# Kernel tuning notes

Hardware: AMD Instinct MI355X
Metric: run time of the kernel (lower is better)

The kernel has to match this reference:

```python
import jax, jax.numpy as jnp
import numpy as np

B, S, H = 16, 384, 768
DK, ESS, WHOLE = 64, 6, 8
HEADER = WHOLE + 1
NL_RGAT = 2


def _sinusoidal_pos(seq_len, dim):
    pos = np.arange(seq_len)[:, None]
    j = np.arange(dim)[None, :]
    enc = pos / np.power(10000.0, 2 * (j // 2) / dim)
    sent = dim // 2
    out = np.zeros((seq_len, dim), dtype=np.float32)
    out[:, :sent] = np.sin(enc[:, 0::2])
    out[:, sent:] = np.cos(enc[:, 1::2])
    return jnp.asarray(out)[None, None]  # [1,1,S,dim]


def _rope(pos, x):
    sin, cos = jnp.split(pos, 2, axis=-1)
    sin_pos = jnp.stack([sin, sin], -1).reshape(pos.shape)
    cos_pos = jnp.stack([cos, cos], -1).reshape(pos.shape)
    rot = jnp.stack([-x[..., 1::2], x[..., 0::2]], -1).reshape(x.shape)
    return x * cos_pos + rot * sin_pos


def _mlp(x, rep_w, rep_b, sc_w, sc_b):
    return jax.nn.relu(x @ rep_w.T + rep_b) @ sc_w.T + sc_b


def _heads(y, mask, n_heads):
    b, s = y.shape[:2]
    return (y * mask).reshape(b, s, n_heads, DK).transpose(0, 2, 1, 3)


def _shaking(M, rows, cols):
    # M: [B,nH,S,S] -> [B,P,nH]; upper triangle (incl diag), row-major
    return M[:, :, rows, cols].transpose(0, 2, 1)


def _layernorm(x, eps=1e-5):
    m = x.mean(-1, keepdims=True)
    v = ((x - m) ** 2).mean(-1, keepdims=True)
    return (x - m) * jax.lax.rsqrt(v + eps)


def setup_inputs() -> dict:
    key = jax.random.key(0)
    ks = jax.random.split(key, 32)
    n = lambda i, shape: jax.random.normal(ks[i], shape, dtype=jnp.float32) * 0.02
    ig = (H + DK * HEADER) // 2          # 672
    ip = (2 * H + DK * ESS) // 2          # 960
    return dict(
        seq_hiddens=jax.random.normal(ks[0], (B, S, H), dtype=jnp.float32),
        attention_mask=jnp.ones((B, S, 1), dtype=jnp.float32),
        wq4gt_w=n(1, (DK, H)), wq4gt_b=n(2, (DK,)),
        wk4gt_w=n(3, (DK, H)), wk4gt_b=n(4, (DK,)),
        wq4g_rep_w=n(5, (ig, H)), wq4g_rep_b=n(6, (ig,)),
        wq4g_sc_w=n(7, (DK * HEADER, ig)), wq4g_sc_b=n(8, (DK * HEADER,)),
        wk4g_rep_w=n(9, (ig, H)), wk4g_rep_b=n(10, (ig,)),
        wk4g_sc_w=n(11, (DK * HEADER, ig)), wk4g_sc_b=n(12, (DK * HEADER,)),
        rgat_w=n(13, (NL_RGAT, HEADER, H, H)),
        wq4t_w=n(14, (DK, 2 * H)), wq4t_b=n(15, (DK,)),
        wk4t_w=n(16, (DK, 2 * H)), wk4t_b=n(17, (DK,)),
        wq_rep_w=n(18, (ip, 2 * H)), wq_rep_b=n(19, (ip,)),
        wq_sc_w=n(20, (DK * ESS, ip)), wq_sc_b=n(21, (DK * ESS,)),
        wk_rep_w=n(22, (ip, 2 * H)), wk_rep_b=n(23, (ip,)),
        wk_sc_w=n(24, (DK * ESS, ip)), wk_sc_b=n(25, (DK * ESS,)),
    )


def reference(seq_hiddens, attention_mask,
              wq4gt_w, wq4gt_b, wk4gt_w, wk4gt_b,
              wq4g_rep_w, wq4g_rep_b, wq4g_sc_w, wq4g_sc_b,
              wk4g_rep_w, wk4g_rep_b, wk4g_sc_w, wk4g_sc_b,
              rgat_w,
              wq4t_w, wq4t_b, wk4t_w, wk4t_b,
              wq_rep_w, wq_rep_b, wq_sc_w, wq_sc_b,
              wk_rep_w, wk_rep_b, wk_sc_w, wk_sc_b):
    pos = _sinusoidal_pos(S, DK)
    rows, cols = np.triu_indices(S)
    inv = 1.0 / np.sqrt(DK).astype(np.float32)
    mask = attention_mask
    x = seq_hiddens

    # ----- graph layer (graph_stack_num = 1) -----
    tsq = _rope(pos, _heads(x @ wq4gt_w.T + wq4gt_b, mask, 1))
    tsk = _rope(pos, _heads(x @ wk4gt_w.T + wk4gt_b, mask, 1))
    thr_g = jax.nn.relu(_shaking(jnp.einsum('bhqd,bhkd->bhqk', tsq, tsk) * inv, rows, cols))

    q = _rope(pos, _heads(_mlp(x, wq4g_rep_w, wq4g_rep_b, wq4g_sc_w, wq4g_sc_b), mask, HEADER))
    k = _rope(pos, _heads(_mlp(x, wk4g_rep_w, wk4g_rep_b, wk4g_sc_w, wk4g_sc_b), mask, HEADER))
    score = jnp.einsum('bhqd,bhkd->bhqk', q, k) * inv  # [B,HEADER,S,S]
    sc_g = _shaking(score[:, :WHOLE], rows, cols)

    upper = jnp.triu(score, 1)
    diag = jnp.triu(score, 0) - upper
    att = upper + jnp.swapaxes(upper, -1, -2) + diag  # symmetric
    adj = jax.nn.softmax(att, -1) * (att != 0)

    feat = x
    for l in range(NL_RGAT):
        hr = jnp.einsum('bsh,roh->brso', feat, rgat_w[l])           # per-relation Linear (no bias)
        agg = jax.nn.relu(jnp.einsum('brst,brto->brso', adj, hr))   # adjacency bmm + ReLU
        feat = _layernorm(jax.nn.relu(agg.sum(1)) / HEADER)         # (dropout is eval-identity)

    # ----- prediction head -----
    inp = jnp.concatenate([seq_hiddens, feat], -1)  # [B,S,2H]
    tq = _rope(pos, _heads(inp @ wq4t_w.T + wq4t_b, mask, 1))
    tk = _rope(pos, _heads(inp @ wk4t_w.T + wk4t_b, mask, 1))
    thr_p = jax.nn.relu(_shaking(jnp.einsum('bhqd,bhkd->bhqk', tq, tk) * inv, rows, cols))

    qp = _rope(pos, _heads(_mlp(inp, wq_rep_w, wq_rep_b, wq_sc_w, wq_sc_b), mask, ESS))
    kp = _rope(pos, _heads(_mlp(inp, wk_rep_w, wk_rep_b, wk_sc_w, wk_sc_b), mask, ESS))
    sc_p = _shaking(jnp.einsum('bhqd,bhkd->bhqk', qp, kp) * inv, rows, cols)

    # concat all shaking outputs along last dim: [B, S(S+1)/2, ESS+1+WHOLE+1]
    return jnp.concatenate([sc_p, thr_p, sc_g, thr_g], -1)
```

## Files before the change

kernel.cpp:

```cpp
#include <hip/hip_runtime.h>
#include <math.h>

typedef unsigned short ushort_t;
typedef __attribute__((ext_vector_type(8))) short short8;
typedef __attribute__((ext_vector_type(4))) float f32x4;

constexpr int B = 16, S = 384, H = 768;
constexpr int BS = B * S;
constexpr long long PAIRS = (long long)S * (S + 1) / 2;
constexpr float INV = 0.125f;

__device__ __forceinline__ ushort_t f2bf(float f) {
  unsigned int u = __float_as_uint(f);
  u += 0x7FFF + ((u >> 16) & 1);
  return (ushort_t)(u >> 16);
}
__device__ __forceinline__ float bf2f(ushort_t u) {
  return __uint_as_float(((unsigned int)u) << 16);
}

__device__ __forceinline__ void glds16(const ushort_t* g, ushort_t* l) {
  __builtin_amdgcn_global_load_lds(
      (const __attribute__((address_space(1))) unsigned int*)g,
      (__attribute__((address_space(3))) unsigned int*)l, 16, 0, 0);
}

__global__ __launch_bounds__(256) void setup_kernel(
    float* tab,
    const float* g_repq, const float* g_repk, const float* g_gtq, const float* g_gtk,
    const float* p_repq, const float* p_repk, const float* p_gtq, const float* p_gtk,
    const float* g_scq, const float* g_sck, const float* p_scq, const float* p_sck,
    float* bqkg, float* bqkp, float* bscg, float* bscp) {
  int b = blockIdx.x;
  if (b < 48) {
    int s = b * 8 + (threadIdx.x >> 5);
    int i = threadIdx.x & 31;
    double ang = (double)s / pow(10000.0, (double)i / 32.0);
    tab[s * 64 + 2 * i]     = (float)cos(ang);
    tab[s * 64 + 2 * i + 1] = (float)sin(ang);
  } else {
    int t = (b - 48) * 256 + threadIdx.x;
    if (t < 1472)
      bqkg[t] = t < 672 ? g_repq[t] : t < 1344 ? g_repk[t - 672]
              : t < 1408 ? g_gtq[t - 1344] : g_gtk[t - 1408];
    if (t < 2048)
      bqkp[t] = t < 960 ? p_repq[t] : t < 1920 ? p_repk[t - 960]
              : t < 1984 ? p_gtq[t - 1920] : p_gtk[t - 1984];
    if (t < 1152) bscg[t] = t < 576 ? g_scq[t] : g_sck[t - 576];
    if (t < 768)  bscp[t] = t < 384 ? p_scq[t] : p_sck[t - 384];
  }
}

constexpr int NJOBS = 14;
struct CvtJobs {
  const float* src[NJOBS];
  ushort_t* dst[NJOBS];
  int n_real[NJOBS];
  int n_tot[NJOBS];
  int blk_off[NJOBS + 1];
};
__global__ __launch_bounds__(256) void cvt_jobs_kernel(CvtJobs J) {
  int blk = blockIdx.x;
  int j = 0;
  while (j < NJOBS - 1 && blk >= J.blk_off[j + 1]) ++j;
  int i4 = (blk - J.blk_off[j]) * 256 + threadIdx.x;
  if (i4 * 4 >= J.n_tot[j]) return;
  ushort4 o;
  if (i4 * 4 < J.n_real[j]) {
    float4 v = ((const float4*)J.src[j])[i4];
    o = make_ushort4(f2bf(v.x), f2bf(v.y), f2bf(v.z), f2bf(v.w));
  } else {
    o = make_ushort4(0, 0, 0, 0);
  }
  ((ushort4*)J.dst[j])[i4] = o;
}

template <int ACT, int CMODE, int SWZ>
__global__ __launch_bounds__(256) void gemm_nt_mfma(
    const ushort_t* __restrict__ A, const ushort_t* __restrict__ W,
    const float* __restrict__ bias, void* __restrict__ Cv,
    ushort_t* __restrict__ pl, ushort_t* __restrict__ qd,
    ushort_t* __restrict__ kd, int cbase, int nsplit,
    int N, int K, int lda, int ldw, int ldc, float alpha, int nh,
    long long sAb, long long sAh, long long sWb, long long sWh,
    long long sCb, long long sCh,
    const float* __restrict__ mask, const float* __restrict__ tab, int biasN) {
  constexpr int SHSZ = (CMODE == 2 || CMODE == 8) ? 17408 : 16384;
  __shared__ __align__(16) ushort_t SH[SHSZ];
  int bx = blockIdx.x, by = blockIdx.y, bz = blockIdx.z;
  if (SWZ) {
    const int nx = gridDim.x, ny = gridDim.y;
    const int nwg = nx * ny * gridDim.z;
    const int hw = bx + nx * (by + ny * bz);
    int l = (hw & 7) * (nwg >> 3) + (hw >> 3);
    const int pz = l / (nx * ny);
    int l2 = l - pz * (nx * ny);
    const int GM = 8;
    const int band = l2 / (GM * nx);
    const int rem = l2 - band * (GM * nx);
    const int gm = (ny - band * GM < GM) ? (ny - band * GM) : GM;
    bx = rem / gm;
    by = band * GM + (rem - bx * gm);
    bz = pz;
  }
  const int zb = bz / nh, zh = bz - zb * nh;
  A += zb * sAb + zh * sAh;
  W += zb * sWb + zh * sWh;
  const int t = threadIdx.x;
  int m0, n0;
  if (CMODE == 3 || CMODE == 8) {
    const int ti = (bx < 3) ? 0 : (bx < 5 ? 1 : 2);
    const int tj = (bx < 3) ? bx : (bx < 5 ? bx - 2 : 2);
    m0 = ti * 128; n0 = tj * 128;
  } else {
    m0 = by * 128; n0 = bx * 128;
  }
  const int lane = t & 63, wid = t >> 6;
  const int wr = wid >> 1, wc = wid & 1;
  const int lrow = lane & 15, lk = lane >> 4;
  const int srow = t >> 2, sch = (t & 3) * 8;
  const ushort_t* Ag = A + (size_t)(m0 + srow) * lda + sch;
  const ushort_t* Wg = W + (size_t)(n0 + srow) * ldw + sch;
  const size_t a64 = (size_t)64 * lda, w64 = (size_t)64 * ldw;

  f32x4 acc[4][4];
#pragma unroll
  for (int i = 0; i < 4; ++i)
#pragma unroll
    for (int j = 0; j < 4; ++j) acc[i][j] = (f32x4){0.f, 0.f, 0.f, 0.f};

  auto stage = [&](int k0, int buf) {
    const int ao = buf * 4096, bo = 8192 + buf * 4096;
    glds16(Ag + k0, &SH[ao + t * 8]);
    glds16(Ag + k0 + a64, &SH[ao + 2048 + t * 8]);
    glds16(Wg + k0, &SH[bo + t * 8]);
    glds16(Wg + k0 + w64, &SH[bo + 2048 + t * 8]);
  };

  const int nk = K >> 5;
  stage(0, 0);
  for (int s = 0; s < nk; ++s) {
    __syncthreads();
    if (s + 1 < nk) stage((s + 1) << 5, (s + 1) & 1);
    const int ao = (s & 1) * 4096, bo = 8192 + (s & 1) * 4096;
    short8 av[4], bv[4];
#pragma unroll
    for (int i = 0; i < 4; ++i) {
      av[i] = *(const short8*)&SH[ao + (wr * 64 + i * 16 + lrow) * 32 + lk * 8];
      bv[i] = *(const short8*)&SH[bo + (wc * 64 + i * 16 + lrow) * 32 + lk * 8];
    }
#pragma unroll
    for (int i = 0; i < 4; ++i)
#pragma unroll
      for (int j = 0; j < 4; ++j)
        acc[i][j] = __builtin_amdgcn_mfma_f32_16x16x32_bf16(av[i], bv[j],
                                                            acc[i][j], 0, 0, 0);
  }

  if (CMODE == 2) {
    __syncthreads();
    const int bb = m0 / S;
    ushort_t* Cb = (ushort_t*)Cv + (size_t)bb * sCb;
    const int s_base = m0 - bb * S;
#pragma unroll
    for (int i = 0; i < 4; ++i) {
      const int sl = wr * 64 + i * 16 + lk * 4;
#pragma unroll
      for (int j = 0; j < 4; ++j) {
        const int nl = wc * 64 + j * 16 + lrow;
        ushort4 o = make_ushort4(f2bf(acc[i][j][0]), f2bf(acc[i][j][1]),
                                 f2bf(acc[i][j][2]), f2bf(acc[i][j][3]));
        *(ushort4*)&SH[nl * 136 + sl] = o;
      }
    }
    __syncthreads();
#pragma unroll
    for (int it = 0; it < 8; ++it) {
      const int row = it * 16 + wid * 4 + lk;
      ushort_t* dst = Cb + (size_t)(n0 + row) * ldc + s_base + lrow * 8;
      *(short8*)dst = *(const short8*)&SH[row * 136 + lrow * 8];
    }
  } else if (CMODE == 3) {
    ushort_t* plc = pl + ((size_t)(cbase + zh) * B + zb) * PAIRS;
#pragma unroll
    for (int j = 0; j < 4; ++j) {
      const int n = n0 + wc * 64 + j * 16 + lrow;
#pragma unroll
      for (int i = 0; i < 4; ++i) {
#pragma unroll
        for (int e = 0; e < 4; ++e) {
          const int m = m0 + wr * 64 + i * 16 + lk * 4 + e;
          if (n >= m) {
            long long p = (long long)m * S - (long long)m * (m - 1) / 2 + (n - m);
            float v = alpha * acc[i][j][e];
            if (ACT == 1) v = fmaxf(v, 0.f);
            plc[p] = f2bf(v);
          }
        }
      }
    }
  } else if (CMODE == 5) {
    ushort_t* Cq = qd + (size_t)zh * sCh;
    const float* bz2 = bias + (size_t)zh * biasN;
#pragma unroll
    for (int j = 0; j < 4; ++j) {
      const int n = n0 + wc * 64 + j * 16 + lrow;
      const float vb = (n < N) ? bz2[n] : 0.f;
      const int d = n & 63;
      const int ti2 = d & ~1;
#pragma unroll
      for (int i = 0; i < 4; ++i) {
#pragma unroll
        for (int e = 0; e < 4; ++e) {
          const int m = m0 + wr * 64 + i * 16 + lk * 4 + e;
          const int s = m % S;
          float v = (n < N) ? (acc[i][j][e] + vb) : 0.f;
          float pv = __shfl_xor(v, 1);
          float c = tab[s * 64 + ti2], sn = tab[s * 64 + ti2 + 1];
          float o = (d & 1) ? (v * c + pv * sn) : (v * c - pv * sn);
          o *= mask[m];
          if (n < N) Cq[(size_t)m * ldc + n] = f2bf(o);
        }
      }
    }
  } else if (CMODE == 6) {
    ushort_t* Cu = (ushort_t*)Cv;
#pragma unroll
    for (int j = 0; j < 4; ++j) {
      const int n = n0 + wc * 64 + j * 16 + lrow;
      const float vb = (n < N) ? bias[n] : 0.f;
#pragma unroll
      for (int i = 0; i < 4; ++i) {
#pragma unroll
        for (int e = 0; e < 4; ++e) {
          const int m = m0 + wr * 64 + i * 16 + lk * 4 + e;
          float v = (n < N) ? (acc[i][j][e] + vb) : 0.f;
          float pv = __shfl_xor(v, 1);
          if (n < nsplit) {
            Cu[(size_t)m * ldc + n] = f2bf(fmaxf(v, 0.f));
          } else if (n < N) {
            const int d = n - nsplit;
            const int dd = d & 63;
            const int ti2 = dd & ~1;
            const int s = m % S;
            float c = tab[s * 64 + ti2], sn = tab[s * 64 + ti2 + 1];
            float o = (dd & 1) ? (v * c + pv * sn) : (v * c - pv * sn);
            o *= mask[m];
            if (d < 64) qd[(size_t)m * 64 + dd] = f2bf(o);
            else        kd[(size_t)m * 64 + dd] = f2bf(o);
          }
        }
      }
    }
  } else if (CMODE == 8) {
    ushort_t* Cu = (ushort_t*)Cv + zb * sCb + zh * sCh;
    ushort_t* plc = pl + ((size_t)(cbase + zh) * B + zb) * PAIRS;
    const bool diag = (m0 == n0);
#pragma unroll
    for (int j = 0; j < 4; ++j) {
      const int n = n0 + wc * 64 + j * 16 + lrow;
#pragma unroll
      for (int i = 0; i < 4; ++i) {
#pragma unroll
        for (int e = 0; e < 4; ++e) {
          const int m = m0 + wr * 64 + i * 16 + lk * 4 + e;
          float v = alpha * acc[i][j][e];
          ushort_t vb = f2bf(v);
          if (!diag || n >= m) Cu[(size_t)m * ldc + n] = vb;
          if (zh < 8 && n >= m) {
            long long p = (long long)m * S - (long long)m * (m - 1) / 2 + (n - m);
            plc[p] = vb;
          }
        }
      }
    }
    __syncthreads();
#pragma unroll
    for (int i = 0; i < 4; ++i) {
      const int sl = wr * 64 + i * 16 + lk * 4;
#pragma unroll
      for (int j = 0; j < 4; ++j) {
        const int nl = wc * 64 + j * 16 + lrow;
        ushort4 o4 = make_ushort4(f2bf(alpha * acc[i][j][0]),
                                  f2bf(alpha * acc[i][j][1]),
                                  f2bf(alpha * acc[i][j][2]),
                                  f2bf(alpha * acc[i][j][3]));
        *(ushort4*)&SH[nl * 136 + sl] = o4;
      }
    }
    __syncthreads();
#pragma unroll
    for (int it = 0; it < 8; ++it) {
      const int rowN = it * 16 + wid * 4 + lk;
      const int colM = lrow * 8;
      if (!diag) {
        *(short8*)&Cu[(size_t)(n0 + rowN) * ldc + m0 + colM] =
            *(const short8*)&SH[rowN * 136 + colM];
      } else {
#pragma unroll
        for (int q = 0; q < 8; ++q)
          if (rowN > colM + q)
            Cu[(size_t)(n0 + rowN) * ldc + m0 + colM + q] =
                SH[rowN * 136 + colM + q];
      }
    }
  }
}

__global__ __launch_bounds__(256) void adj_bmm_kernel(
    const ushort_t* __restrict__ adjb, const ushort_t* __restrict__ hrt,
    ushort_t* __restrict__ Q0, ushort_t* __restrict__ Q1,
    ushort_t* __restrict__ Q2, ushort_t* __restrict__ Q3,
    ushort_t* __restrict__ Q4) {
  __shared__ __align__(16) ushort_t As[2][128 * 32];
  __shared__ __align__(16) ushort_t Bs[2][128 * 32];
  int bx = blockIdx.x, by = blockIdx.y, bz = blockIdx.z;
  {
    int nx = gridDim.x, ny = gridDim.y;
    int nwg = nx * ny * gridDim.z;
    int flat = bx + nx * (by + ny * bz);
    int l = (flat & 7) * (nwg >> 3) + (flat >> 3);
    bx = l % nx; l /= nx; by = l % ny; bz = l / ny;
  }
  const int b = bz / 5, rg = bz - b * 5;
  ushort_t* Q = (rg == 0) ? Q0 : (rg == 1) ? Q1 : (rg == 2) ? Q2
              : (rg == 3) ? Q3 : Q4;
  const int rel0 = (rg < 4) ? rg * 2 : 8;
  const int nsteps = (rg < 4) ? 24 : 12;
  const int t = threadIdx.x;
  const int m0 = by * 128, n0 = bx * 128;
  const int lane = t & 63, wid = t >> 6;
  const int wr = wid >> 1, wc = wid & 1;
  const int lrow = lane & 15, lk = lane >> 4;
  const int srow = t >> 2, sch = (t & 3) * 8;

  const ushort_t* adjA =
      adjb + ((size_t)(b * 9 + rel0) * S + m0 + srow) * S + sch;
  const ushort_t* hrA =
      hrt + ((size_t)(b * 9 + rel0) * H + n0 + srow) * S + sch;

  float mac[4][4][4];
#pragma unroll
  for (int i = 0; i < 4; ++i)
#pragma unroll
    for (int j = 0; j < 4; ++j)
#pragma unroll
      for (int e = 0; e < 4; ++e) mac[i][j][e] = 0.f;

  f32x4 acc[4][4];
#pragma unroll
  for (int i = 0; i < 4; ++i)
#pragma unroll
    for (int j = 0; j < 4; ++j) acc[i][j] = (f32x4){0.f, 0.f, 0.f, 0.f};

  auto stage = [&](int s, int buf) {
    const int rr = s / 12;
    const int k0 = (s - rr * 12) * 32;
    const ushort_t* Ag = adjA + (size_t)rr * S * S + k0;
    const ushort_t* Wg = hrA + (size_t)rr * H * S + k0;
    glds16(Ag, &As[buf][t * 8]);
    glds16(Ag + 64 * S, &As[buf][2048 + t * 8]);
    glds16(Wg, &Bs[buf][t * 8]);
    glds16(Wg + 64 * S, &Bs[buf][2048 + t * 8]);
  };

  stage(0, 0);
  for (int s = 0; s < nsteps; ++s) {
    __syncthreads();
    if (s + 1 < nsteps) stage(s + 1, (s + 1) & 1);
    const int buf = s & 1;
    short8 av[4], bv[4];
#pragma unroll
    for (int i = 0; i < 4; ++i) {
      av[i] = *(const short8*)&As[buf][(wr * 64 + i * 16 + lrow) * 32 + lk * 8];
      bv[i] = *(const short8*)&Bs[buf][(wc * 64 + i * 16 + lrow) * 32 + lk * 8];
    }
#pragma unroll
    for (int i = 0; i < 4; ++i)
#pragma unroll
      for (int j = 0; j < 4; ++j)
        acc[i][j] = __builtin_amdgcn_mfma_f32_16x16x32_bf16(av[i], bv[j],
                                                            acc[i][j], 0, 0, 0);
    if ((s % 12) == 11) {
#pragma unroll
      for (int i = 0; i < 4; ++i)
#pragma unroll
        for (int j = 0; j < 4; ++j) {
#pragma unroll
          for (int e = 0; e < 4; ++e)
            mac[i][j][e] += fmaxf(acc[i][j][e], 0.f);
          acc[i][j] = (f32x4){0.f, 0.f, 0.f, 0.f};
        }
    }
  }

#pragma unroll
  for (int i = 0; i < 4; ++i)
#pragma unroll
    for (int j = 0; j < 4; ++j)
#pragma unroll
      for (int e = 0; e < 4; ++e) {
        const int m = m0 + wr * 64 + i * 16 + lk * 4 + e;
        const int n = n0 + wc * 64 + j * 16 + lrow;
        Q[((size_t)b * S + m) * H + n] = f2bf(mac[i][j][e]);
      }
}

__global__ __launch_bounds__(128) void softmax_mask_kernel(
    const ushort_t* __restrict__ Mt, ushort_t* __restrict__ adjb) {
  __shared__ float red[128];
  int row = blockIdx.x;
  const ushort_t* r = Mt + (size_t)row * S;
  ushort_t* o = adjb + (size_t)row * S;
  int t = threadIdx.x;
  const bool act = t < 96;
  float v[4];
  float mx = -INFINITY;
  if (act) {
    ushort4 u = ((const ushort4*)r)[t];
    v[0] = bf2f(u.x); v[1] = bf2f(u.y); v[2] = bf2f(u.z); v[3] = bf2f(u.w);
    mx = fmaxf(fmaxf(v[0], v[1]), fmaxf(v[2], v[3]));
  }
  red[t] = mx; __syncthreads();
  for (int off2 = 64; off2 > 0; off2 >>= 1) {
    if (t < off2) red[t] = fmaxf(red[t], red[t + off2]);
    __syncthreads();
  }
  mx = red[0]; __syncthreads();
  float e4[4], s = 0.f;
  if (act) {
#pragma unroll
    for (int q = 0; q < 4; ++q) { e4[q] = expf(v[q] - mx); s += e4[q]; }
  }
  red[t] = s; __syncthreads();
  for (int off2 = 64; off2 > 0; off2 >>= 1) {
    if (t < off2) red[t] += red[t + off2];
    __syncthreads();
  }
  float invs = 1.f / red[0];
  if (act) {
    ushort4 ou;
    ou.x = f2bf((v[0] != 0.f) ? e4[0] * invs : 0.f);
    ou.y = f2bf((v[1] != 0.f) ? e4[1] * invs : 0.f);
    ou.z = f2bf((v[2] != 0.f) ? e4[2] * invs : 0.f);
    ou.w = f2bf((v[3] != 0.f) ? e4[3] * invs : 0.f);
    ((ushort4*)o)[t] = ou;
  }
}

__global__ __launch_bounds__(256) void ln_finalize_kernel(
    const ushort_t* __restrict__ Q0, const ushort_t* __restrict__ Q1,
    const ushort_t* __restrict__ Q2, const ushort_t* __restrict__ Q3,
    const ushort_t* __restrict__ Q4, const ushort_t* __restrict__ xb,
    ushort_t* __restrict__ inp) {
  __shared__ float red[256];
  int row = blockIdx.x;
  const size_t base = (size_t)row * H;
  ushort_t* xrow = inp + (size_t)row * (2 * H);
  ushort_t* fb = xrow + H;
  int t = threadIdx.x;
  float v[3];
  float s = 0.f;
#pragma unroll
  for (int q = 0; q < 3; ++q) {
    size_t ix = base + t + q * 256;
    v[q] = (bf2f(Q0[ix]) + bf2f(Q1[ix]) + bf2f(Q2[ix]) + bf2f(Q3[ix]) +
            bf2f(Q4[ix])) / 9.0f;
    s += v[q];
  }
  red[t] = s; __syncthreads();
#pragma unroll
  for (int q = 0; q < 3; ++q)
    xrow[t + q * 256] = xb[base + t + q * 256];
  for (int off2 = 128; off2 > 0; off2 >>= 1) {
    if (t < off2) red[t] += red[t + off2];
    __syncthreads();
  }
  float mean = red[0] / (float)H; __syncthreads();
  float s2 = 0.f;
#pragma unroll
  for (int q = 0; q < 3; ++q) { float d = v[q] - mean; s2 += d * d; }
  red[t] = s2; __syncthreads();
  for (int off2 = 128; off2 > 0; off2 >>= 1) {
    if (t < off2) red[t] += red[t + off2];
    __syncthreads();
  }
  float var = red[0] / (float)H;
  float rs = rsqrtf(var + 1e-5f);
#pragma unroll
  for (int q = 0; q < 3; ++q)
    fb[t + q * 256] = f2bf((v[q] - mean) * rs);
}

__global__ __launch_bounds__(256) void gather16_kernel(
    const ushort_t* __restrict__ plA, const ushort_t* __restrict__ plB,
    float* __restrict__ out) {
  int idx = blockIdx.x * 256 + threadIdx.x;
  if (idx >= (int)(B * PAIRS)) return;
  const size_t PLN = (size_t)B * PAIRS;
  float v[16];
#pragma unroll
  for (int ch = 0; ch < 7; ++ch)  v[ch] = bf2f(plA[(size_t)ch * PLN + idx]);
#pragma unroll
  for (int ch = 7; ch < 16; ++ch) v[ch] = bf2f(plB[(size_t)(ch - 7) * PLN + idx]);
  float4* dst = (float4*)(out + (size_t)idx * 16);
#pragma unroll
  for (int q = 0; q < 4; ++q)
    dst[q] = make_float4(v[4 * q], v[4 * q + 1], v[4 * q + 2], v[4 * q + 3]);
}

extern "C" void kernel_launch(void* const* d_in, const int* in_sizes, int n_in,
                              void* d_out, int out_size, void* d_ws, size_t ws_size,
                              hipStream_t stream) {
  (void)in_sizes; (void)n_in; (void)out_size; (void)ws_size;
  const float* x          = (const float*)d_in[0];
  const float* mask       = (const float*)d_in[1];
  const float* wq4gt_w    = (const float*)d_in[2];
  const float* wq4gt_b    = (const float*)d_in[3];
  const float* wk4gt_w    = (const float*)d_in[4];
  const float* wk4gt_b    = (const float*)d_in[5];
  const float* wq4g_rep_w = (const float*)d_in[6];
  const float* wq4g_rep_b = (const float*)d_in[7];
  const float* wq4g_sc_w  = (const float*)d_in[8];
  const float* wq4g_sc_b  = (const float*)d_in[9];
  const float* wk4g_rep_w = (const float*)d_in[10];
  const float* wk4g_rep_b = (const float*)d_in[11];
  const float* wk4g_sc_w  = (const float*)d_in[12];
  const float* wk4g_sc_b  = (const float*)d_in[13];
  const float* rgat_w     = (const float*)d_in[14];
  const float* wq4t_w     = (const float*)d_in[15];
  const float* wq4t_b     = (const float*)d_in[16];
  const float* wk4t_w     = (const float*)d_in[17];
  const float* wk4t_b     = (const float*)d_in[18];
  const float* wq_rep_w   = (const float*)d_in[19];
  const float* wq_rep_b   = (const float*)d_in[20];
  const float* wq_sc_w    = (const float*)d_in[21];
  const float* wq_sc_b    = (const float*)d_in[22];
  const float* wk_rep_w   = (const float*)d_in[23];
  const float* wk_rep_b   = (const float*)d_in[24];
  const float* wk_sc_w    = (const float*)d_in[25];
  const float* wk_sc_b    = (const float*)d_in[26];
  float* out = (float*)d_out;

  char* wsb = (char*)d_ws;
  size_t off = 0;
  auto af = [&](size_t n) { float* p = (float*)(wsb + off);
                            off += ((n * 4 + 255) & ~(size_t)255); return p; };
  auto au = [&](size_t n) { ushort_t* p = (ushort_t*)(wsb + off);
                            off += ((n * 2 + 255) & ~(size_t)255); return p; };

  float* t_rope = af(24576);
  float* t_scg  = af((size_t)B * 9 * S * S);
  float* t_acc  = af((size_t)BS * H);
  ushort_t* xb    = au((size_t)BS * H);
  ushort_t* inpb  = au((size_t)BS * 2 * H);
  ushort_t* repb  = au((size_t)BS * 1920);
  ushort_t* qb    = au((size_t)BS * 576);
  ushort_t* kb    = au((size_t)BS * 576);
  ushort_t* adjb  = au((size_t)B * 9 * S * S);
  ushort_t* plB   = au((size_t)9 * B * PAIRS);
  ushort_t* wqkg  = au(1179648);
  ushort_t* wqkp  = au(3145728);
  ushort_t* wq4g_scb = au(430080);
  ushort_t* wk4g_scb = au(430080);
  ushort_t* wq_scb   = au(368640);
  ushort_t* wk_scb   = au(368640);
  ushort_t* rgatb    = au(10616832);
  float* bqkg = af(1472);
  float* bqkp = af(2048);
  float* bscg = af(1152);
  float* bscp = af(768);

  ushort_t* scg_u = (ushort_t*)t_scg;
  ushort_t* hr_t  = (ushort_t*)t_scg;
  ushort_t* plA   = rgatb;
  ushort_t* Q0 = (ushort_t*)t_acc;
  ushort_t* Q1 = Q0 + (size_t)BS * H;
  ushort_t* Q2 = repb;
  ushort_t* Q3 = Q2 + (size_t)BS * H;
  ushort_t* Q4 = qb;

  setup_kernel<<<56, 256, 0, stream>>>(
      t_rope,
      wq4g_rep_b, wk4g_rep_b, wq4gt_b, wk4gt_b,
      wq_rep_b, wk_rep_b, wq4t_b, wk4t_b,
      wq4g_sc_b, wk4g_sc_b, wq_sc_b, wk_sc_b,
      bqkg, bqkp, bscg, bscp);

  {
    CvtJobs J;
    const float* srcs[NJOBS] = {wq4g_rep_w, wk4g_rep_w, wq4gt_w, wk4gt_w,
                                wq_rep_w, wk_rep_w, wq4t_w, wk4t_w,
                                wq4g_sc_w, wk4g_sc_w, wq_sc_w, wk_sc_w,
                                rgat_w, x};
    ushort_t* dsts[NJOBS] = {wqkg, wqkg + 516096, wqkg + 1032192, wqkg + 1081344,
                             wqkp, wqkp + 1474560, wqkp + 2949120, wqkp + 3047424,
                             wq4g_scb, wk4g_scb, wq_scb, wk_scb,
                             rgatb, xb};
    int nreal[NJOBS] = {516096, 516096, 49152, 49152,
                        1474560, 1474560, 98304, 98304,
                        387072, 387072, 368640, 368640,
                        10616832, 4718592};
    int ntot[NJOBS]  = {516096, 516096, 49152, 98304,
                        1474560, 1474560, 98304, 98304,
                        430080, 430080, 368640, 368640,
                        10616832, 4718592};
    int acc_blk = 0;
    for (int j = 0; j < NJOBS; ++j) {
      J.src[j] = srcs[j]; J.dst[j] = dsts[j];
      J.n_real[j] = nreal[j]; J.n_tot[j] = ntot[j];
      J.blk_off[j] = acc_blk;
      acc_blk += (ntot[j] + 1023) / 1024;
    }
    J.blk_off[NJOBS] = acc_blk;
    cvt_jobs_kernel<<<acc_blk, 256, 0, stream>>>(J);
  }

  gemm_nt_mfma<0, 6, 1><<<dim3(12, 48, 1), 256, 0, stream>>>(
      xb, wqkg, bqkg, repb, nullptr, qb, kb, 0, 1344,
      1472, 768, 768, 768, 1344, 1.f, 1, 0, 0, 0, 0, 0, 0,
      mask, t_rope, 0);
  gemm_nt_mfma<1, 3, 1><<<dim3(6, 1, B), 256, 0, stream>>>(
      qb, kb, nullptr, nullptr, plB, nullptr, nullptr, 8, 0,
      S, 64, 64, 64, 0, INV, 1,
      (long long)S * 64, 0, (long long)S * 64, 0, 0, 0,
      nullptr, nullptr, 0);

  gemm_nt_mfma<0, 5, 1><<<dim3(5, 48, 2), 256, 0, stream>>>(
      repb, wq4g_scb, bscg, nullptr, nullptr, qb, nullptr, 0, 0,
      576, 672, 1344, 672, 576, 1.f, 2,
      0, 672, 0, 430080, 0, (long long)BS * 576,
      mask, t_rope, 576);
  gemm_nt_mfma<0, 8, 1><<<dim3(6, 1, B * 9), 256, 0, stream>>>(
      qb, kb, nullptr, scg_u, plB, nullptr, nullptr, 0, 0,
      S, 64, 576, 576, S, INV, 9,
      (long long)S * 576, 64, (long long)S * 576, 64,
      (long long)9 * S * S, (long long)S * S,
      nullptr, nullptr, 0);
  softmax_mask_kernel<<<B * 9 * S, 128, 0, stream>>>(scg_u, adjb);

  for (int l = 0; l < 2; ++l) {
    const ushort_t* fsrc = (l == 0) ? xb : inpb + H;
    const int flda = (l == 0) ? H : 2 * H;
    gemm_nt_mfma<0, 2, 1><<<dim3(54, 48, 1), 256, 0, stream>>>(
        fsrc, rgatb + (size_t)l * 9 * H * H, nullptr, hr_t, nullptr, nullptr,
        nullptr, 0, 0,
        9 * H, H, flda, H, S, 1.f, 1, 0, 0, 0, 0, (long long)9 * H * S, 0,
        nullptr, nullptr, 0);
    adj_bmm_kernel<<<dim3(6, 3, B * 5), 256, 0, stream>>>(
        adjb, hr_t, Q0, Q1, Q2, Q3, Q4);
    ln_finalize_kernel<<<BS, 256, 0, stream>>>(Q0, Q1, Q2, Q3, Q4, xb, inpb);
  }

  gemm_nt_mfma<0, 6, 1><<<dim3(16, 48, 1), 256, 0, stream>>>(
      inpb, wqkp, bqkp, repb, nullptr, qb, kb, 0, 1920,
      2048, 1536, 1536, 1536, 1920, 1.f, 1, 0, 0, 0, 0, 0, 0,
      mask, t_rope, 0);
  gemm_nt_mfma<1, 3, 1><<<dim3(6, 1, B), 256, 0, stream>>>(
      qb, kb, nullptr, nullptr, plA, nullptr, nullptr, 6, 0,
      S, 64, 64, 64, 0, INV, 1,
      (long long)S * 64, 0, (long long)S * 64, 0, 0, 0,
      nullptr, nullptr, 0);

  gemm_nt_mfma<0, 5, 1><<<dim3(3, 48, 2), 256, 0, stream>>>(
      repb, wq_scb, bscp, nullptr, nullptr, qb, nullptr, 0, 0,
      384, 960, 1920, 960, 384, 1.f, 2,
      0, 960, 0, 368640, 0, (long long)BS * 384,
      mask, t_rope, 384);
  gemm_nt_mfma<0, 3, 1><<<dim3(6, 1, B * 6), 256, 0, stream>>>(
      qb, qb + (size_t)BS * 384, nullptr, nullptr, plA, nullptr, nullptr, 0, 0,
      S, 64, 384, 384, 0, INV, 6,
      (long long)S * 384, 64, (long long)S * 384, 64, 0, 0,
      nullptr, nullptr, 0);

  gather16_kernel<<<(int)((B * PAIRS + 255) / 256), 256, 0, stream>>>(plA, plB, out);
}
```

Baseline: 654.0 us.

## Merge setup into convert kernel and co-launch independent small GEMMs

Folds the RoPE-table and bias-packing setup into the weight-conversion kernel so both run as one launch. Redirects the global-token q/k projections to spare buffers so the small triangular score GEMM can share a launch with the independent sc-projection GEMM, through a new dual-dispatch kernel driven by a flat block index. This cuts launch count and lets the under-filled 96-block GEMM overlap with the larger one. In exchange, kernel arguments now go through a struct and the merged kernels may use more registers or LDS.

Result: faster. 637.6 us (-2.5%).

```diff
diff --git a/kernel.cpp b/kernel.cpp
--- a/kernel.cpp
+++ b/kernel.cpp
@@ -23,32 +23,6 @@
   __builtin_amdgcn_global_load_lds(
       (const __attribute__((address_space(1))) unsigned int*)g,
       (__attribute__((address_space(3))) unsigned int*)l, 16, 0, 0);
-}
-
-__global__ __launch_bounds__(256) void setup_kernel(
-    float* tab,
-    const float* g_repq, const float* g_repk, const float* g_gtq, const float* g_gtk,
-    const float* p_repq, const float* p_repk, const float* p_gtq, const float* p_gtk,
-    const float* g_scq, const float* g_sck, const float* p_scq, const float* p_sck,
-    float* bqkg, float* bqkp, float* bscg, float* bscp) {
-  int b = blockIdx.x;
-  if (b < 48) {
-    int s = b * 8 + (threadIdx.x >> 5);
-    int i = threadIdx.x & 31;
-    double ang = (double)s / pow(10000.0, (double)i / 32.0);
-    tab[s * 64 + 2 * i]     = (float)cos(ang);
-    tab[s * 64 + 2 * i + 1] = (float)sin(ang);
-  } else {
-    int t = (b - 48) * 256 + threadIdx.x;
-    if (t < 1472)
-      bqkg[t] = t < 672 ? g_repq[t] : t < 1344 ? g_repk[t - 672]
-              : t < 1408 ? g_gtq[t - 1344] : g_gtk[t - 1408];
-    if (t < 2048)
-      bqkp[t] = t < 960 ? p_repq[t] : t < 1920 ? p_repk[t - 960]
-              : t < 1984 ? p_gtq[t - 1920] : p_gtk[t - 1984];
-    if (t < 1152) bscg[t] = t < 576 ? g_scq[t] : g_sck[t - 576];
-    if (t < 768)  bscp[t] = t < 384 ? p_scq[t] : p_sck[t - 384];
-  }
 }
 
 constexpr int NJOBS = 14;
@@ -59,8 +33,34 @@
   int n_tot[NJOBS];
   int blk_off[NJOBS + 1];
 };
-__global__ __launch_bounds__(256) void cvt_jobs_kernel(CvtJobs J) {
+__global__ __launch_bounds__(256) void cvt_setup_kernel(
+    CvtJobs J, int cvtBlocks, float* tab,
+    const float* g_repq, const float* g_repk, const float* g_gtq, const float* g_gtk,
+    const float* p_repq, const float* p_repk, const float* p_gtq, const float* p_gtk,
+    const float* g_scq, const float* g_sck, const float* p_scq, const float* p_sck,
+    float* bqkg, float* bqkp, float* bscg, float* bscp) {
   int blk = blockIdx.x;
+  if (blk >= cvtBlocks) {
+    int b = blk - cvtBlocks;
+    if (b < 48) {
+      int s = b * 8 + (threadIdx.x >> 5);
+      int i = threadIdx.x & 31;
+      double ang = (double)s / pow(10000.0, (double)i / 32.0);
+      tab[s * 64 + 2 * i]     = (float)cos(ang);
+      tab[s * 64 + 2 * i + 1] = (float)sin(ang);
+    } else {
+      int t = (b - 48) * 256 + threadIdx.x;
+      if (t < 1472)
+        bqkg[t] = t < 672 ? g_repq[t] : t < 1344 ? g_repk[t - 672]
+                : t < 1408 ? g_gtq[t - 1344] : g_gtk[t - 1408];
+      if (t < 2048)
+        bqkp[t] = t < 960 ? p_repq[t] : t < 1920 ? p_repk[t - 960]
+                : t < 1984 ? p_gtq[t - 1920] : p_gtk[t - 1984];
+      if (t < 1152) bscg[t] = t < 576 ? g_scq[t] : g_sck[t - 576];
+      if (t < 768)  bscp[t] = t < 384 ? p_scq[t] : p_sck[t - 384];
+    }
+    return;
+  }
   int j = 0;
   while (j < NJOBS - 1 && blk >= J.blk_off[j + 1]) ++j;
   int i4 = (blk - J.blk_off[j]) * 256 + threadIdx.x;
@@ -75,24 +75,24 @@
   ((ushort4*)J.dst[j])[i4] = o;
 }
 
-template <int ACT, int CMODE, int SWZ>
-__global__ __launch_bounds__(256) void gemm_nt_mfma(
-    const ushort_t* __restrict__ A, const ushort_t* __restrict__ W,
-    const float* __restrict__ bias, void* __restrict__ Cv,
-    ushort_t* __restrict__ pl, ushort_t* __restrict__ qd,
-    ushort_t* __restrict__ kd, int cbase, int nsplit,
-    int N, int K, int lda, int ldw, int ldc, float alpha, int nh,
-    long long sAb, long long sAh, long long sWb, long long sWh,
-    long long sCb, long long sCh,
-    const float* __restrict__ mask, const float* __restrict__ tab, int biasN) {
+struct GemmArgs {
+  const ushort_t* A; const ushort_t* W; const float* bias; void* Cv;
+  ushort_t* pl; ushort_t* qd; ushort_t* kd; int cbase, nsplit;
+  int N, K, lda, ldw, ldc; float alpha; int nh;
+  long long sAb, sAh, sWb, sWh, sCb, sCh;
+  const float* mask; const float* tab; int biasN;
+  int nx, ny, nz;
+};
+
+template <int ACT, int CMODE>
+__device__ void gemm_body(const GemmArgs g, int flat) {
   constexpr int SHSZ = (CMODE == 2 || CMODE == 8) ? 17408 : 16384;
   __shared__ __align__(16) ushort_t SH[SHSZ];
-  int bx = blockIdx.x, by = blockIdx.y, bz = blockIdx.z;
-  if (SWZ) {
-    const int nx = gridDim.x, ny = gridDim.y;
-    const int nwg = nx * ny * gridDim.z;
-    const int hw = bx + nx * (by + ny * bz);
-    int l = (hw & 7) * (nwg >> 3) + (hw >> 3);
+  const int nx = g.nx, ny = g.ny;
+  int bx, by, bz;
+  {
+    const int nwg = nx * ny * g.nz;
+    int l = (flat & 7) * (nwg >> 3) + (flat >> 3);
     const int pz = l / (nx * ny);
     int l2 = l - pz * (nx * ny);
     const int GM = 8;
@@ -103,9 +103,9 @@
     by = band * GM + (rem - bx * gm);
     bz = pz;
   }
-  const int zb = bz / nh, zh = bz - zb * nh;
-  A += zb * sAb + zh * sAh;
-  W += zb * sWb + zh * sWh;
+  const int zb = bz / g.nh, zh = bz - zb * g.nh;
+  const ushort_t* A = g.A + zb * g.sAb + zh * g.sAh;
+  const ushort_t* W = g.W + zb * g.sWb + zh * g.sWh;
   const int t = threadIdx.x;
   int m0, n0;
   if (CMODE == 3 || CMODE == 8) {
@@ -119,6 +119,7 @@
   const int wr = wid >> 1, wc = wid & 1;
   const int lrow = lane & 15, lk = lane >> 4;
   const int srow = t >> 2, sch = (t & 3) * 8;
+  const int lda = g.lda, ldw = g.ldw, ldc = g.ldc;
   const ushort_t* Ag = A + (size_t)(m0 + srow) * lda + sch;
   const ushort_t* Wg = W + (size_t)(n0 + srow) * ldw + sch;
   const size_t a64 = (size_t)64 * lda, w64 = (size_t)64 * ldw;
@@ -137,7 +138,7 @@
     glds16(Wg + k0 + w64, &SH[bo + 2048 + t * 8]);
   };
 
-  const int nk = K >> 5;
+  const int nk = g.K >> 5;
   stage(0, 0);
   for (int s = 0; s < nk; ++s) {
     __syncthreads();
@@ -160,7 +161,7 @@
   if (CMODE == 2) {
     __syncthreads();
     const int bb = m0 / S;
-    ushort_t* Cb = (ushort_t*)Cv + (size_t)bb * sCb;
+    ushort_t* Cb = (ushort_t*)g.Cv + (size_t)bb * g.sCb;
     const int s_base = m0 - bb * S;
 #pragma unroll
     for (int i = 0; i < 4; ++i) {
@@ -181,7 +182,7 @@
       *(short8*)dst = *(const short8*)&SH[row * 136 + lrow * 8];
     }
   } else if (CMODE == 3) {
-    ushort_t* plc = pl + ((size_t)(cbase + zh) * B + zb) * PAIRS;
+    ushort_t* plc = g.pl + ((size_t)(g.cbase + zh) * B + zb) * PAIRS;
 #pragma unroll
     for (int j = 0; j < 4; ++j) {
       const int n = n0 + wc * 64 + j * 16 + lrow;
@@ -192,7 +193,7 @@
           const int m = m0 + wr * 64 + i * 16 + lk * 4 + e;
           if (n >= m) {
             long long p = (long long)m * S - (long long)m * (m - 1) / 2 + (n - m);
-            float v = alpha * acc[i][j][e];
+            float v = g.alpha * acc[i][j][e];
             if (ACT == 1) v = fmaxf(v, 0.f);
             plc[p] = f2bf(v);
           }
@@ -200,12 +201,12 @@
       }
     }
   } else if (CMODE == 5) {
-    ushort_t* Cq = qd + (size_t)zh * sCh;
-    const float* bz2 = bias + (size_t)zh * biasN;
+    ushort_t* Cq = g.qd + (size_t)zh * g.sCh;
+    const float* bz2 = g.bias + (size_t)zh * g.biasN;
 #pragma unroll
     for (int j = 0; j < 4; ++j) {
       const int n = n0 + wc * 64 + j * 16 + lrow;
-      const float vb = (n < N) ? bz2[n] : 0.f;
+      const float vb = (n < g.N) ? bz2[n] : 0.f;
       const int d = n & 63;
       const int ti2 = d & ~1;
 #pragma unroll
@@ -214,47 +215,47 @@
         for (int e = 0; e < 4; ++e) {
           const int m = m0 + wr * 64 + i * 16 + lk * 4 + e;
           const int s = m % S;
-          float v = (n < N) ? (acc[i][j][e] + vb) : 0.f;
+          float v = (n < g.N) ? (acc[i][j][e] + vb) : 0.f;
           float pv = __shfl_xor(v, 1);
-          float c = tab[s * 64 + ti2], sn = tab[s * 64 + ti2 + 1];
+          float c = g.tab[s * 64 + ti2], sn = g.tab[s * 64 + ti2 + 1];
           float o = (d & 1) ? (v * c + pv * sn) : (v * c - pv * sn);
-          o *= mask[m];
-          if (n < N) Cq[(size_t)m * ldc + n] = f2bf(o);
+          o *= g.mask[m];
+          if (n < g.N) Cq[(size_t)m * ldc + n] = f2bf(o);
         }
       }
     }
   } else if (CMODE == 6) {
-    ushort_t* Cu = (ushort_t*)Cv;
+    ushort_t* Cu = (ushort_t*)g.Cv;
 #pragma unroll
     for (int j = 0; j < 4; ++j) {
       const int n = n0 + wc * 64 + j * 16 + lrow;
-      const float vb = (n < N) ? bias[n] : 0.f;
+      const float vb = (n < g.N) ? g.bias[n] : 0.f;
 #pragma unroll
       for (int i = 0; i < 4; ++i) {
 #pragma unroll
         for (int e = 0; e < 4; ++e) {
           const int m = m0 + wr * 64 + i * 16 + lk * 4 + e;
-          float v = (n < N) ? (acc[i][j][e] + vb) : 0.f;
+          float v = (n < g.N) ? (acc[i][j][e] + vb) : 0.f;
           float pv = __shfl_xor(v, 1);
-          if (n < nsplit) {
+          if (n < g.nsplit) {
             Cu[(size_t)m * ldc + n] = f2bf(fmaxf(v, 0.f));
-          } else if (n < N) {
-            const int d = n - nsplit;
+          } else if (n < g.N) {
+            const int d = n - g.nsplit;
             const int dd = d & 63;
             const int ti2 = dd & ~1;
             const int s = m % S;
-            float c = tab[s * 64 + ti2], sn = tab[s * 64 + ti2 + 1];
+            float c = g.tab[s * 64 + ti2], sn = g.tab[s * 64 + ti2 + 1];
             float o = (dd & 1) ? (v * c + pv * sn) : (v * c - pv * sn);
-            o *= mask[m];
-            if (d < 64) qd[(size_t)m * 64 + dd] = f2bf(o);
-            else        kd[(size_t)m * 64 + dd] = f2bf(o);
+            o *= g.mask[m];
+            if (d < 64) g.qd[(size_t)m * 64 + dd] = f2bf(o);
+            else        g.kd[(size_t)m * 64 + dd] = f2bf(o);
           }
         }
       }
     }
   } else if (CMODE == 8) {
-    ushort_t* Cu = (ushort_t*)Cv + zb * sCb + zh * sCh;
-    ushort_t* plc = pl + ((size_t)(cbase + zh) * B + zb) * PAIRS;
+    ushort_t* Cu = (ushort_t*)g.Cv + zb * g.sCb + zh * g.sCh;
+    ushort_t* plc = g.pl + ((size_t)(g.cbase + zh) * B + zb) * PAIRS;
     const bool diag = (m0 == n0);
 #pragma unroll
     for (int j = 0; j < 4; ++j) {
@@ -264,7 +265,7 @@
 #pragma unroll
         for (int e = 0; e < 4; ++e) {
           const int m = m0 + wr * 64 + i * 16 + lk * 4 + e;
-          float v = alpha * acc[i][j][e];
+          float v = g.alpha * acc[i][j][e];
           ushort_t vb = f2bf(v);
           if (!diag || n >= m) Cu[(size_t)m * ldc + n] = vb;
           if (zh < 8 && n >= m) {
@@ -281,10 +282,10 @@
 #pragma unroll
       for (int j = 0; j < 4; ++j) {
         const int nl = wc * 64 + j * 16 + lrow;
-        ushort4 o4 = make_ushort4(f2bf(alpha * acc[i][j][0]),
-                                  f2bf(alpha * acc[i][j][1]),
-                                  f2bf(alpha * acc[i][j][2]),
-                                  f2bf(alpha * acc[i][j][3]));
+        ushort4 o4 = make_ushort4(f2bf(g.alpha * acc[i][j][0]),
+                                  f2bf(g.alpha * acc[i][j][1]),
+                                  f2bf(g.alpha * acc[i][j][2]),
+                                  f2bf(g.alpha * acc[i][j][3]));
         *(ushort4*)&SH[nl * 136 + sl] = o4;
       }
     }
@@ -305,6 +306,18 @@
       }
     }
   }
+}
+
+template <int ACT, int CMODE>
+__global__ __launch_bounds__(256) void gemm_one(GemmArgs g) {
+  gemm_body<ACT, CMODE>(g, blockIdx.x + g.nx * (blockIdx.y + g.ny * blockIdx.z));
+}
+
+template <int ACTA, int CMA, int ACTB, int CMB>
+__global__ __launch_bounds__(256) void gemm_dual(GemmArgs a, GemmArgs b, int nA) {
+  int f = blockIdx.x;
+  if (f < nA) gemm_body<ACTA, CMA>(a, f);
+  else        gemm_body<ACTB, CMB>(b, f - nA);
 }
 
 __global__ __launch_bounds__(256) void adj_bmm_kernel(
@@ -574,18 +587,13 @@
   ushort_t* scg_u = (ushort_t*)t_scg;
   ushort_t* hr_t  = (ushort_t*)t_scg;
   ushort_t* plA   = rgatb;
+  ushort_t* gtq   = adjb;
+  ushort_t* gtk   = adjb + (size_t)BS * 64;
   ushort_t* Q0 = (ushort_t*)t_acc;
   ushort_t* Q1 = Q0 + (size_t)BS * H;
   ushort_t* Q2 = repb;
   ushort_t* Q3 = Q2 + (size_t)BS * H;
   ushort_t* Q4 = qb;
-
-  setup_kernel<<<56, 256, 0, stream>>>(
-      t_rope,
-      wq4g_rep_b, wk4g_rep_b, wq4gt_b, wk4gt_b,
-      wq_rep_b, wk_rep_b, wq4t_b, wk4t_b,
-      wq4g_sc_b, wk4g_sc_b, wq_sc_b, wk_sc_b,
-      bqkg, bqkp, bscg, bscp);
 
   {
     CvtJobs J;
@@ -613,65 +621,81 @@
       acc_blk += (ntot[j] + 1023) / 1024;
     }
     J.blk_off[NJOBS] = acc_blk;
-    cvt_jobs_kernel<<<acc_blk, 256, 0, stream>>>(J);
-  }
-
-  gemm_nt_mfma<0, 6, 1><<<dim3(12, 48, 1), 256, 0, stream>>>(
-      xb, wqkg, bqkg, repb, nullptr, qb, kb, 0, 1344,
+    cvt_setup_kernel<<<acc_blk + 56, 256, 0, stream>>>(
+        J, acc_blk, t_rope,
+        wq4g_rep_b, wk4g_rep_b, wq4gt_b, wk4gt_b,
+        wq_rep_b, wk_rep_b, wq4t_b, wk4t_b,
+        wq4g_sc_b, wk4g_sc_b, wq_sc_b, wk_sc_b,
+        bqkg, bqkp, bscg, bscp);
+  }
+
+  auto GA = [](const ushort_t* A, const ushort_t* W, const float* bias, void* Cv,
+               ushort_t* pl, ushort_t* qd, ushort_t* kd, int cbase, int nsplit,
+               int N, int K, int lda, int ldw, int ldc, float alpha, int nh,
+               long long sAb, long long sAh, long long sWb, long long sWh,
+               long long sCb, long long sCh,
+               const float* mask, const float* tab, int biasN,
+               int nx, int ny, int nz) {
+    GemmArgs g{A, W, bias, Cv, pl, qd, kd, cbase, nsplit,
+               N, K, lda, ldw, ldc, alpha, nh,
+               sAb, sAh, sWb, sWh, sCb, sCh, mask, tab, biasN, nx, ny, nz};
+    return g;
+  };
+
+  gemm_one<0, 6><<<dim3(12, 48, 1), 256, 0, stream>>>(GA(
+      xb, wqkg, bqkg, repb, nullptr, gtq, gtk, 0, 1344,
       1472, 768, 768, 768, 1344, 1.f, 1, 0, 0, 0, 0, 0, 0,
-      mask, t_rope, 0);
-  gemm_nt_mfma<1, 3, 1><<<dim3(6, 1, B), 256, 0, stream>>>(
-      qb, kb, nullptr, nullptr, plB, nullptr, nullptr, 8, 0,
-      S, 64, 64, 64, 0, INV, 1,
-      (long long)S * 64, 0, (long long)S * 64, 0, 0, 0,
-      nullptr, nullptr, 0);
-
-  gemm_nt_mfma<0, 5, 1><<<dim3(5, 48, 2), 256, 0, stream>>>(
-      repb, wq4g_scb, bscg, nullptr, nullptr, qb, nullptr, 0, 0,
-      576, 672, 1344, 672, 576, 1.f, 2,
-      0, 672, 0, 430080, 0, (long long)BS * 576,
-      mask, t_rope, 576);
-  gemm_nt_mfma<0, 8, 1><<<dim3(6, 1, B * 9), 256, 0, stream>>>(
+      mask, t_rope, 0, 12, 48, 1));
+  gemm_dual<1, 3, 0, 5><<<96 + 480, 256, 0, stream>>>(
+      GA(gtq, gtk, nullptr, nullptr, plB, nullptr, nullptr, 8, 0,
+         S, 64, 64, 64, 0, INV, 1,
+         (long long)S * 64, 0, (long long)S * 64, 0, 0, 0,
+         nullptr, nullptr, 0, 6, 1, B),
+      GA(repb, wq4g_scb, bscg, nullptr, nullptr, qb, nullptr, 0, 0,
+         576, 672, 1344, 672, 576, 1.f, 2,
+         0, 672, 0, 430080, 0, (long long)BS * 576,
+         mask, t_rope, 576, 5, 48, 2),
+      96);
+  gemm_one<0, 8><<<dim3(6, 1, B * 9), 256, 0, stream>>>(GA(
       qb, kb, nullptr, scg_u, plB, nullptr, nullptr, 0, 0,
       S, 64, 576, 576, S, INV, 9,
       (long long)S * 576, 64, (long long)S * 576, 64,
       (long long)9 * S * S, (long long)S * S,
-      nullptr, nullptr, 0);
+      nullptr, nullptr, 0, 6, 1, B * 9));
   softmax_mask_kernel<<<B * 9 * S, 128, 0, stream>>>(scg_u, adjb);
 
   for (int l = 0; l < 2; ++l) {
     const ushort_t* fsrc = (l == 0) ? xb : inpb + H;
     const int flda = (l == 0) ? H : 2 * H;
-    gemm_nt_mfma<0, 2, 1><<<dim3(54, 48, 1), 256, 0, stream>>>(
+    gemm_one<0, 2><<<dim3(54, 48, 1), 256, 0, stream>>>(GA(
         fsrc, rgatb + (size_t)l * 9 * H * H, nullptr, hr_t, nullptr, nullptr,
         nullptr, 0, 0,
         9 * H, H, flda, H, S, 1.f, 1, 0, 0, 0, 0, (long long)9 * H * S, 0,
-        nullptr, nullptr, 0);
+        nullptr, nullptr, 0, 54, 48, 1));
     adj_bmm_kernel<<<dim3(6, 3, B * 5), 256, 0, stream>>>(
         adjb, hr_t, Q0, Q1, Q2, Q3, Q4);
     ln_finalize_kernel<<<BS, 256, 0, stream>>>(Q0, Q1, Q2, Q3, Q4, xb, inpb);
   }
 
-  gemm_nt_mfma<0, 6, 1><<<dim3(16, 48, 1), 256, 0, stream>>>(
-      inpb, wqkp, bqkp, repb, nullptr, qb, kb, 0, 1920,
+  gemm_one<0, 6><<<dim3(16, 48, 1), 256, 0, stream>>>(GA(
+      inpb, wqkp, bqkp, repb, nullptr, gtq, gtk, 0, 1920,
       2048, 1536, 1536, 1536, 1920, 1.f, 1, 0, 0, 0, 0, 0, 0,
-      mask, t_rope, 0);
-  gemm_nt_mfma<1, 3, 1><<<dim3(6, 1, B), 256, 0, stream>>>(
-      qb, kb, nullptr, nullptr, plA, nullptr, nullptr, 6, 0,
-      S, 64, 64, 64, 0, INV, 1,
-      (long long)S * 64, 0, (long long)S * 64, 0, 0, 0,
-      nullptr, nullptr, 0);
-
-  gemm_nt_mfma<0, 5, 1><<<dim3(3, 48, 2), 256, 0, stream>>>(
-      repb, wq_scb, bscp, nullptr, nullptr, qb, nullptr, 0, 0,
-      384, 960, 1920, 960, 384, 1.f, 2,
-      0, 960, 0, 368640, 0, (long long)BS * 384,
-      mask, t_rope, 384);
-  gemm_nt_mfma<0, 3, 1><<<dim3(6, 1, B * 6), 256, 0, stream>>>(
+      mask, t_rope, 0, 16, 48, 1));
+  gemm_dual<1, 3, 0, 5><<<96 + 288, 256, 0, stream>>>(
+      GA(gtq, gtk, nullptr, nullptr, plA, nullptr, nullptr, 6, 0,
+         S, 64, 64, 64, 0, INV, 1,
+         (long long)S * 64, 0, (long long)S * 64, 0, 0, 0,
+         nullptr, nullptr, 0, 6, 1, B),
+      GA(repb, wq_scb, bscp, nullptr, nullptr, qb, nullptr, 0, 0,
+         384, 960, 1920, 960, 384, 1.f, 2,
+         0, 960, 0, 368640, 0, (long long)BS * 384,
+         mask, t_rope, 384, 3, 48, 2),
+      96);
+  gemm_one<0, 3><<<dim3(6, 1, B * 6), 256, 0, stream>>>(GA(
       qb, qb + (size_t)BS * 384, nullptr, nullptr, plA, nullptr, nullptr, 0, 0,
       S, 64, 384, 384, 0, INV, 6,
       (long long)S * 384, 64, (long long)S * 384, 64, 0, 0,
-      nullptr, nullptr, 0);
+      nullptr, nullptr, 0, 6, 1, B * 6));
 
   gather16_kernel<<<(int)((B * PAIRS + 255) / 256), 256, 0, stream>>>(plA, plB, out);
 }
```
